# Performance work log

Hardware: AMD Instinct MI355X
Metric: run time of the kernel (lower is better)

Reference implementation:

```python
import jax, jax.numpy as jnp
import numpy as np

B, S, D = 1024, 192, 512
MAX_ITEMS, NUM_LAYERS = 64, 3
LN_EPS = 1e-5


def setup_inputs() -> dict:
    key = jax.random.key(0)
    k_tok, k_pad, k_item, k_layer, k_temp = jax.random.split(key, 5)
    token_embeddings = jax.random.normal(k_tok, (B, S, D), dtype=jnp.float32)
    # Left-padded mask: zeros then contiguous ones until the end of the row.
    pad_len = jax.random.randint(k_pad, (B,), 0, S)  # at least 1 real token
    attention_mask = (jnp.arange(S)[None, :] >= pad_len[:, None]).astype(jnp.int32)
    item_pos_emb = 0.01 * jax.random.normal(k_item, (MAX_ITEMS, D), dtype=jnp.float32)
    layer_emb = 0.01 * jax.random.normal(k_layer, (NUM_LAYERS, D), dtype=jnp.float32)
    temporal_decay = 0.02 * jax.random.normal(k_temp, (MAX_ITEMS, D), dtype=jnp.float32)
    ln_weight = jnp.ones((D,), dtype=jnp.float32)
    ln_bias = jnp.zeros((D,), dtype=jnp.float32)
    return {
        "token_embeddings": token_embeddings,
        "attention_mask": attention_mask,
        "item_pos_emb": item_pos_emb,
        "layer_emb": layer_emb,
        "temporal_decay": temporal_decay,
        "ln_weight": ln_weight,
        "ln_bias": ln_bias,
    }


def reference(token_embeddings, attention_mask, item_pos_emb, layer_emb,
              temporal_decay, ln_weight, ln_bias):
    mask = attention_mask > 0                              # (B, S) bool
    has_content = jnp.any(mask, axis=1)                    # (B,)
    start = jnp.argmax(mask, axis=1)                       # first non-pad index
    end = S - jnp.argmax(mask[:, ::-1], axis=1)            # last non-pad index + 1
    idx = jnp.arange(S)[None, :]                           # (1, S)
    pos = idx - start[:, None]                             # content-relative position
    in_range = (pos >= 0) & (idx < end[:, None]) & has_content[:, None]
    pos_c = jnp.clip(pos, 0)
    item_idx = jnp.where(in_range, pos_c // NUM_LAYERS, 0)  # (B, S)
    layer_idx = jnp.where(in_range, pos_c % NUM_LAYERS, 0)
    add = item_pos_emb[item_idx] + layer_emb[layer_idx] + temporal_decay[item_idx]
    enhanced = token_embeddings + jnp.where(in_range[..., None], add, 0.0)
    # LayerNorm over last dim
    mu = jnp.mean(enhanced, axis=-1, keepdims=True)
    var = jnp.mean(jnp.square(enhanced - mu), axis=-1, keepdims=True)
    normed = (enhanced - mu) * jax.lax.rsqrt(var + LN_EPS) * ln_weight + ln_bias
    # zero out padding (dropout is identity in eval mode)
    return normed * attention_mask[..., None].astype(normed.dtype)
```

## Files before the change

### kernel.cpp

```cpp
#include <hip/hip_runtime.h>

#define BB 1024
#define SS 192
#define DD 512
#define NUM_LAYERS 3
#define LN_EPS 1e-5f

__global__ void start_kernel(const int* __restrict__ mask, int* __restrict__ start) {
    int b = blockIdx.x * blockDim.x + threadIdx.x;
    if (b >= BB) return;
    const int* m = mask + b * SS;
    int st = 0;
    for (int i = SS - 1; i >= 0; --i) {
        if (m[i] > 0) st = i;
    }
    start[b] = st;
}

__global__ __launch_bounds__(128) void fused_kernel(
    const float* __restrict__ tok,
    const int* __restrict__ mask,
    const float* __restrict__ item_pos,
    const float* __restrict__ layer_emb,
    const float* __restrict__ decay,
    const float* __restrict__ lnw,
    const float* __restrict__ lnb,
    const int* __restrict__ start,
    float* __restrict__ out)
{
    const int row = blockIdx.x;
    const int b = row / SS;
    const int s = row - b * SS;
    const int t = threadIdx.x;

    float* o = out + (size_t)row * DD;

    const int mk = mask[row];
    if (mk == 0) {
        float4 z = make_float4(0.f, 0.f, 0.f, 0.f);
        reinterpret_cast<float4*>(o)[t] = z;
        return;
    }

    const int st = start[b];
    const int pos = s - st;
    const int item_idx = pos / NUM_LAYERS;
    const int layer_idx = pos - item_idx * NUM_LAYERS;

    const float* x = tok + (size_t)row * DD;
    float4 xv = reinterpret_cast<const float4*>(x)[t];

    const float4 a1 = reinterpret_cast<const float4*>(item_pos + item_idx * DD)[t];
    const float4 a2 = reinterpret_cast<const float4*>(layer_emb + layer_idx * DD)[t];
    const float4 a3 = reinterpret_cast<const float4*>(decay + item_idx * DD)[t];

    xv.x += a1.x + a2.x + a3.x;
    xv.y += a1.y + a2.y + a3.y;
    xv.z += a1.z + a2.z + a3.z;
    xv.w += a1.w + a2.w + a3.w;

    float sum = xv.x + xv.y + xv.z + xv.w;
    float sq  = xv.x * xv.x + xv.y * xv.y + xv.z * xv.z + xv.w * xv.w;

    #pragma unroll
    for (int off = 32; off > 0; off >>= 1) {
        sum += __shfl_down(sum, off, 64);
        sq  += __shfl_down(sq,  off, 64);
    }

    __shared__ float2 partial[2];
    const int wave = t >> 6;
    if ((t & 63) == 0) partial[wave] = make_float2(sum, sq);
    __syncthreads();

    const float tsum = partial[0].x + partial[1].x;
    const float tsq  = partial[0].y + partial[1].y;

    const float mu  = tsum * (1.0f / DD);
    const float var = tsq * (1.0f / DD) - mu * mu;
    const float inv = rsqrtf(var + LN_EPS);

    const float4 wv = reinterpret_cast<const float4*>(lnw)[t];
    const float4 bv = reinterpret_cast<const float4*>(lnb)[t];

    float4 ov;
    ov.x = (xv.x - mu) * inv * wv.x + bv.x;
    ov.y = (xv.y - mu) * inv * wv.y + bv.y;
    ov.z = (xv.z - mu) * inv * wv.z + bv.z;
    ov.w = (xv.w - mu) * inv * wv.w + bv.w;

    reinterpret_cast<float4*>(o)[t] = ov;
}

extern "C" void kernel_launch(void* const* d_in, const int* in_sizes, int n_in,
                              void* d_out, int out_size, void* d_ws, size_t ws_size,
                              hipStream_t stream) {
    const float* tok       = (const float*)d_in[0];
    const int*   mask      = (const int*)d_in[1];
    const float* item_pos  = (const float*)d_in[2];
    const float* layer_emb = (const float*)d_in[3];
    const float* decay     = (const float*)d_in[4];
    const float* lnw       = (const float*)d_in[5];
    const float* lnb       = (const float*)d_in[6];
    float* out = (float*)d_out;

    int* start = (int*)d_ws;

    start_kernel<<<(BB + 255) / 256, 256, 0, stream>>>(mask, start);
    fused_kernel<<<BB * SS, 128, 0, stream>>>(tok, mask, item_pos, layer_emb,
                                              decay, lnw, lnb, start, out);
}
```

Measured before the change: 175.7 us.

## Map one wavefront per row and use ballot-based start search

```diff
diff --git a/kernel.cpp b/kernel.cpp
--- a/kernel.cpp
+++ b/kernel.cpp
@@ -6,18 +6,24 @@
 #define NUM_LAYERS 3
 #define LN_EPS 1e-5f
 
-__global__ void start_kernel(const int* __restrict__ mask, int* __restrict__ start) {
-    int b = blockIdx.x * blockDim.x + threadIdx.x;
+__global__ __launch_bounds__(256) void start_kernel(const int* __restrict__ mask,
+                                                    int* __restrict__ start) {
+    const int b = (blockIdx.x * blockDim.x + threadIdx.x) >> 6;
+    const int lane = threadIdx.x & 63;
     if (b >= BB) return;
     const int* m = mask + b * SS;
-    int st = 0;
-    for (int i = SS - 1; i >= 0; --i) {
-        if (m[i] > 0) st = i;
-    }
-    start[b] = st;
+    const unsigned long long b0 = __ballot(m[lane] > 0);
+    const unsigned long long b1 = __ballot(m[lane + 64] > 0);
+    const unsigned long long b2 = __ballot(m[lane + 128] > 0);
+    int idx;
+    if (b0)      idx = __ffsll(b0) - 1;
+    else if (b1) idx = 64 + __ffsll(b1) - 1;
+    else if (b2) idx = 128 + __ffsll(b2) - 1;
+    else         idx = 0;
+    if (lane == 0) start[b] = idx;
 }
 
-__global__ __launch_bounds__(128) void fused_kernel(
+__global__ __launch_bounds__(256) void fused_kernel(
     const float* __restrict__ tok,
     const int* __restrict__ mask,
     const float* __restrict__ item_pos,
@@ -28,17 +34,18 @@
     const int* __restrict__ start,
     float* __restrict__ out)
 {
-    const int row = blockIdx.x;
+    const int wid = threadIdx.x >> 6;
+    const int lane = threadIdx.x & 63;
+    const int row = blockIdx.x * 4 + wid;
     const int b = row / SS;
     const int s = row - b * SS;
-    const int t = threadIdx.x;
 
-    float* o = out + (size_t)row * DD;
+    float4* o4 = reinterpret_cast<float4*>(out + (size_t)row * DD);
 
-    const int mk = mask[row];
-    if (mk == 0) {
-        float4 z = make_float4(0.f, 0.f, 0.f, 0.f);
-        reinterpret_cast<float4*>(o)[t] = z;
+    if (mask[row] == 0) {
+        const float4 z = make_float4(0.f, 0.f, 0.f, 0.f);
+        o4[lane] = z;
+        o4[lane + 64] = z;
         return;
     }
 
@@ -47,49 +54,54 @@
     const int item_idx = pos / NUM_LAYERS;
     const int layer_idx = pos - item_idx * NUM_LAYERS;
 
-    const float* x = tok + (size_t)row * DD;
-    float4 xv = reinterpret_cast<const float4*>(x)[t];
+    const float4* x4 = reinterpret_cast<const float4*>(tok + (size_t)row * DD);
+    float4 xv0 = x4[lane];
+    float4 xv1 = x4[lane + 64];
 
-    const float4 a1 = reinterpret_cast<const float4*>(item_pos + item_idx * DD)[t];
-    const float4 a2 = reinterpret_cast<const float4*>(layer_emb + layer_idx * DD)[t];
-    const float4 a3 = reinterpret_cast<const float4*>(decay + item_idx * DD)[t];
+    const float4* i4 = reinterpret_cast<const float4*>(item_pos + item_idx * DD);
+    const float4* l4 = reinterpret_cast<const float4*>(layer_emb + layer_idx * DD);
+    const float4* d4 = reinterpret_cast<const float4*>(decay + item_idx * DD);
 
-    xv.x += a1.x + a2.x + a3.x;
-    xv.y += a1.y + a2.y + a3.y;
-    xv.z += a1.z + a2.z + a3.z;
-    xv.w += a1.w + a2.w + a3.w;
+    const float4 i0 = i4[lane], i1 = i4[lane + 64];
+    const float4 l0 = l4[lane], l1 = l4[lane + 64];
+    const float4 dd0 = d4[lane], dd1 = d4[lane + 64];
 
-    float sum = xv.x + xv.y + xv.z + xv.w;
-    float sq  = xv.x * xv.x + xv.y * xv.y + xv.z * xv.z + xv.w * xv.w;
+    xv0.x += i0.x + l0.x + dd0.x;  xv0.y += i0.y + l0.y + dd0.y;
+    xv0.z += i0.z + l0.z + dd0.z;  xv0.w += i0.w + l0.w + dd0.w;
+    xv1.x += i1.x + l1.x + dd1.x;  xv1.y += i1.y + l1.y + dd1.y;
+    xv1.z += i1.z + l1.z + dd1.z;  xv1.w += i1.w + l1.w + dd1.w;
+
+    float sum = xv0.x + xv0.y + xv0.z + xv0.w + xv1.x + xv1.y + xv1.z + xv1.w;
+    float sq  = xv0.x * xv0.x + xv0.y * xv0.y + xv0.z * xv0.z + xv0.w * xv0.w
+              + xv1.x * xv1.x + xv1.y * xv1.y + xv1.z * xv1.z + xv1.w * xv1.w;
 
     #pragma unroll
-    for (int off = 32; off > 0; off >>= 1) {
-        sum += __shfl_down(sum, off, 64);
-        sq  += __shfl_down(sq,  off, 64);
+    for (int m = 32; m > 0; m >>= 1) {
+        sum += __shfl_xor(sum, m, 64);
+        sq  += __shfl_xor(sq,  m, 64);
     }
 
-    __shared__ float2 partial[2];
-    const int wave = t >> 6;
-    if ((t & 63) == 0) partial[wave] = make_float2(sum, sq);
-    __syncthreads();
-
-    const float tsum = partial[0].x + partial[1].x;
-    const float tsq  = partial[0].y + partial[1].y;
-
-    const float mu  = tsum * (1.0f / DD);
-    const float var = tsq * (1.0f / DD) - mu * mu;
+    const float mu  = sum * (1.0f / DD);
+    const float var = sq * (1.0f / DD) - mu * mu;
     const float inv = rsqrtf(var + LN_EPS);
 
-    const float4 wv = reinterpret_cast<const float4*>(lnw)[t];
-    const float4 bv = reinterpret_cast<const float4*>(lnb)[t];
+    const float4* w4 = reinterpret_cast<const float4*>(lnw);
+    const float4* bb4 = reinterpret_cast<const float4*>(lnb);
+    const float4 w0 = w4[lane], w1 = w4[lane + 64];
+    const float4 b0 = bb4[lane], b1 = bb4[lane + 64];
 
-    float4 ov;
-    ov.x = (xv.x - mu) * inv * wv.x + bv.x;
-    ov.y = (xv.y - mu) * inv * wv.y + bv.y;
-    ov.z = (xv.z - mu) * inv * wv.z + bv.z;
-    ov.w = (xv.w - mu) * inv * wv.w + bv.w;
+    float4 ov0, ov1;
+    ov0.x = (xv0.x - mu) * inv * w0.x + b0.x;
+    ov0.y = (xv0.y - mu) * inv * w0.y + b0.y;
+    ov0.z = (xv0.z - mu) * inv * w0.z + b0.z;
+    ov0.w = (xv0.w - mu) * inv * w0.w + b0.w;
+    ov1.x = (xv1.x - mu) * inv * w1.x + b1.x;
+    ov1.y = (xv1.y - mu) * inv * w1.y + b1.y;
+    ov1.z = (xv1.z - mu) * inv * w1.z + b1.z;
+    ov1.w = (xv1.w - mu) * inv * w1.w + b1.w;
 
-    reinterpret_cast<float4*>(o)[t] = ov;
+    o4[lane] = ov0;
+    o4[lane + 64] = ov1;
 }
 
 extern "C" void kernel_launch(void* const* d_in, const int* in_sizes, int n_in,
@@ -106,7 +118,7 @@
 
     int* start = (int*)d_ws;
 
-    start_kernel<<<(BB + 255) / 256, 256, 0, stream>>>(mask, start);
-    fused_kernel<<<BB * SS, 128, 0, stream>>>(tok, mask, item_pos, layer_emb,
-                                              decay, lnw, lnb, start, out);
+    start_kernel<<<(BB * 64 + 255) / 256, 256, 0, stream>>>(mask, start);
+    fused_kernel<<<(BB * SS) / 4, 256, 0, stream>>>(tok, mask, item_pos, layer_emb,
+                                                    decay, lnw, lnb, start, out);
 }
```

After: 157.9 us. -10.1%, faster.
